# Kernel optimization log

Hardware: AMD Instinct MI355X
Metric: run time of the kernel (lower is better)

## Reference

```python
import jax, jax.numpy as jnp
import numpy as np

W_NBITS = 4
GROUP_SIZE = 128
ELEMS_PER_SAMPLE = 32 // W_NBITS  # 8 nibbles per int32 word
UNPACK_MASK = (1 << W_NBITS) - 1  # 15

M, K, N = 8192, 4096, 11008
KP = K // ELEMS_PER_SAMPLE        # 512 packed rows
NG = K // GROUP_SIZE              # 32 quantization groups


def setup_inputs() -> dict:
    key = jax.random.key(0)
    k1, k2, k3, k4 = jax.random.split(key, 4)
    x = jax.random.normal(k1, (M, K), dtype=jnp.float32)
    # packed 4-bit weights: 8 nibbles per int32 word, packed over the K dim
    W_q = jax.random.randint(k2, (KP, N), 0, 2147483647, dtype=jnp.int32)
    # group-wise scales (small positive) and zero-points (in [0, 15])
    scales = jax.random.uniform(k3, (NG, N), dtype=jnp.float32) * 0.01 + 1e-4
    zeros = jax.random.uniform(k4, (NG, N), dtype=jnp.float32) * float(UNPACK_MASK)
    return {"x": x, "W_q": W_q, "scales": scales, "zeros": zeros}


def _dequantize(W_q, scales, zeros):
    # Unpack 8 consecutive K-rows from each int32 word: [KP, N] -> [KP, 8, N] -> [K, N]
    shifts = (jnp.arange(ELEMS_PER_SAMPLE, dtype=jnp.int32) * W_NBITS)
    nibbles = (W_q[:, None, :] >> shifts[None, :, None]) & UNPACK_MASK
    W = nibbles.reshape(KP * ELEMS_PER_SAMPLE, N).astype(jnp.float32)
    # W_group_mode=3: (w - zero) * scale, group index g = k // group_size
    sf = jnp.repeat(scales, GROUP_SIZE, axis=0)  # [K, N]
    zf = jnp.repeat(zeros, GROUP_SIZE, axis=0)   # [K, N]
    return (W - zf) * sf


def reference(x, W_q, scales, zeros):
    W_dq = _dequantize(W_q, scales, zeros)  # [K, N]
    return jnp.matmul(x, W_dq)              # [M, N]
```

## Files before the change

kernel.cpp:

```cpp
#include <hip/hip_runtime.h>
#include <stdint.h>

#define M_DIM 8192
#define K_DIM 4096
#define N_DIM 11008
#define KP_DIM 512

#define A_PRE_BYTES (67108864ull)
#define B_PRE_BYTES (90177536ull)
#define WS_NEEDED   (A_PRE_BYTES + B_PRE_BYTES)

typedef __attribute__((ext_vector_type(8))) short bf16x8;
typedef __attribute__((ext_vector_type(4))) float f32x4;

__device__ __forceinline__ uint32_t pack2_bf16(float lo, float hi) {
    uint32_t ulo = (__float_as_uint(lo) + 0x8000u) >> 16;
    uint32_t uhi = (__float_as_uint(hi) + 0x8000u) & 0xFFFF0000u;
    return uhi | ulo;
}

__device__ __forceinline__ uint4 dequant_word(uint32_t w, float s, float b) {
    const uint32_t MG = 0x43000000u, MK = 0x000F0000u;
    float f0 = __uint_as_float(((w << 16) & MK) | MG);
    float f1 = __uint_as_float(((w << 12) & MK) | MG);
    float f2 = __uint_as_float(((w <<  8) & MK) | MG);
    float f3 = __uint_as_float(((w <<  4) & MK) | MG);
    float f4 = __uint_as_float(( w        & MK) | MG);
    float f5 = __uint_as_float(((w >>  4) & MK) | MG);
    float f6 = __uint_as_float(((w >>  8) & MK) | MG);
    float f7 = __uint_as_float(((w >> 12) & MK) | MG);
    uint4 o;
    o.x = pack2_bf16(fmaf(f0, s, b), fmaf(f1, s, b));
    o.y = pack2_bf16(fmaf(f2, s, b), fmaf(f3, s, b));
    o.z = pack2_bf16(fmaf(f4, s, b), fmaf(f5, s, b));
    o.w = pack2_bf16(fmaf(f6, s, b), fmaf(f7, s, b));
    return o;
}


__global__ void conv_x(const float* __restrict__ x, uint32_t* __restrict__ Apre) {
    const int c   = blockIdx.x * 256 + threadIdx.x;
    const int row = blockIdx.y;
    const float4* p = reinterpret_cast<const float4*>(x + (size_t)row * K_DIM + c * 8);
    float4 v0 = p[0], v1 = p[1];
    uint4 o;
    o.x = pack2_bf16(v0.x, v0.y);
    o.y = pack2_bf16(v0.z, v0.w);
    o.z = pack2_bf16(v1.x, v1.y);
    o.w = pack2_bf16(v1.z, v1.w);
    const int m_blk = row >> 7, mt = (row >> 4) & 7, lrow = row & 15;
    const int k_blk = c >> 3, ks = (c >> 2) & 1, q = c & 3;
    const int lane  = (q << 4) | lrow;
    const size_t dst = (((size_t)m_blk * 64 + k_blk) * 16 + mt * 2 + ks) * 64 + lane;
    *reinterpret_cast<uint4*>(Apre + dst * 4) = o;
}

__global__ void dequant_w(const int* __restrict__ Wq, const float* __restrict__ scales,
                          const float* __restrict__ zeros, uint32_t* __restrict__ Bpre) {
    const int n  = blockIdx.x * 256 + threadIdx.x;
    const int kp = blockIdx.y;
    const uint32_t w = (uint32_t)Wq[(size_t)kp * N_DIM + n];
    const int g = kp >> 4;
    const float s = scales[(size_t)g * N_DIM + n];
    const float z = zeros[(size_t)g * N_DIM + n];
    const float b = -(128.0f + z) * s;
    uint4 o = dequant_word(w, s, b);
    const int n_blk = n >> 7, nt = (n >> 4) & 7;
    const int k_blk = kp >> 3, ks = (kp >> 2) & 1, q = kp & 3;
    const int lane  = (q << 4) | (n & 15);
    const size_t dst = (((size_t)n_blk * 64 + k_blk) * 16 + nt * 2 + ks) * 64 + lane;
    *reinterpret_cast<uint4*>(Bpre + dst * 4) = o;
}

#define GLD16(g, l) __builtin_amdgcn_global_load_lds(                        \
    (const __attribute__((address_space(1))) uint32_t*)(g),                  \
    (__attribute__((address_space(3))) uint32_t*)(l), 16, 0, 0)

__global__ __launch_bounds__(256, 2)
void gemm_pre(const uint32_t* __restrict__ Apre, const uint32_t* __restrict__ Bpre,
              float* __restrict__ out) {
    __shared__ uint32_t As[4096];
    __shared__ uint32_t Bs[4096];

    const int tid  = threadIdx.x;
    const int lane = tid & 63;
    const int wv   = tid >> 6;
    const int wm   = wv >> 1, wn = wv & 1;
    const int m_blk = blockIdx.x, n_blk = blockIdx.y;

    const uint32_t* ag = Apre + ((size_t)m_blk * 64 * 16 + wv * 4) * 256 + lane * 4;
    const uint32_t* bg = Bpre + ((size_t)n_blk * 64 * 16 + wv * 4) * 256 + lane * 4;
    uint32_t* al = &As[(wv * 4) * 256];
    uint32_t* bl = &Bs[(wv * 4) * 256];

    f32x4 acc[4][4];
#pragma unroll
    for (int mt = 0; mt < 4; ++mt)
#pragma unroll
        for (int nt = 0; nt < 4; ++nt)
            acc[mt][nt] = (f32x4){0.f, 0.f, 0.f, 0.f};

    for (int kb = 0; kb < 64; ++kb) {
#pragma unroll
        for (int i = 0; i < 4; ++i) {
            GLD16(ag + i * 256, al + i * 256);
            GLD16(bg + i * 256, bl + i * 256);
        }
        ag += 4096;
        bg += 4096;
        __syncthreads();

#pragma unroll
        for (int ks = 0; ks < 2; ++ks) {
            bf16x8 af[4], bfr[4];
#pragma unroll
            for (int mt = 0; mt < 4; ++mt)
                af[mt] = *reinterpret_cast<const bf16x8*>(
                    &As[(((wm * 4 + mt) << 1) | ks) * 256 + lane * 4]);
#pragma unroll
            for (int nt = 0; nt < 4; ++nt)
                bfr[nt] = *reinterpret_cast<const bf16x8*>(
                    &Bs[(((wn * 4 + nt) << 1) | ks) * 256 + lane * 4]);
#pragma unroll
            for (int mt = 0; mt < 4; ++mt)
#pragma unroll
                for (int nt = 0; nt < 4; ++nt)
                    acc[mt][nt] = __builtin_amdgcn_mfma_f32_16x16x32_bf16(
                        af[mt], bfr[nt], acc[mt][nt], 0, 0, 0);
        }
        __syncthreads();
    }

    const int colc = lane & 15, qr = lane >> 4;
#pragma unroll
    for (int mt = 0; mt < 4; ++mt) {
#pragma unroll
        for (int nt = 0; nt < 4; ++nt) {
            int row0 = m_blk * 128 + (wm * 4 + mt) * 16 + qr * 4;
            int c    = n_blk * 128 + (wn * 4 + nt) * 16 + colc;
#pragma unroll
            for (int i = 0; i < 4; ++i)
                out[(size_t)(row0 + i) * N_DIM + c] = acc[mt][nt][i];
        }
    }
}

__global__ __launch_bounds__(256, 2)
void qgemm_fused(const float* __restrict__ x, const int* __restrict__ Wq,
                 const float* __restrict__ scales, const float* __restrict__ zeros,
                 float* __restrict__ out) {
    __shared__ uint32_t As[4096];
    __shared__ uint32_t Bs[4096];

    const int tid  = threadIdx.x;
    const int lane = tid & 63;
    const int wv   = tid >> 6;
    const int wm   = wv >> 1, wn = wv & 1;
    const int m0 = blockIdx.x * 128;
    const int n0 = blockIdx.y * 128;
    const int bc  = tid & 127;
    const int brh = tid >> 7;

    int a_row[4], a_col[4], a_dst[4];
#pragma unroll
    for (int j = 0; j < 4; ++j) {
        int sl  = tid + 256 * j;
        int blk = sl >> 6;
        int ln  = sl & 63;
        int mt  = blk >> 1, ks = blk & 1;
        a_row[j] = m0 + mt * 16 + (ln & 15);
        a_col[j] = ks * 32 + (ln >> 4) * 8;
        a_dst[j] = blk * 256 + ln * 4;
    }

    f32x4 acc[4][4];
#pragma unroll
    for (int mt = 0; mt < 4; ++mt)
#pragma unroll
        for (int nt = 0; nt < 4; ++nt)
            acc[mt][nt] = (f32x4){0.f, 0.f, 0.f, 0.f};

    float4   pa[4][2];
    uint32_t pw[4];
    float    s_raw, z_raw;
#pragma unroll
    for (int j = 0; j < 4; ++j) {
        const float4* p = reinterpret_cast<const float4*>(
            x + (size_t)a_row[j] * K_DIM + a_col[j]);
        pa[j][0] = p[0];
        pa[j][1] = p[1];
    }
#pragma unroll
    for (int j = 0; j < 4; ++j) {
        int r = brh * 4 + j;
        pw[j] = (uint32_t)Wq[(size_t)r * N_DIM + n0 + bc];
    }
    s_raw = scales[n0 + bc];
    z_raw = zeros[n0 + bc];

    float sv = 0.f, bv = 0.f;

    for (int kk = 0; kk < K_DIM; kk += 64) {
        if ((kk & 127) == 0) {
            sv = s_raw;
            bv = -(128.0f + z_raw) * s_raw;
        }
#pragma unroll
        for (int j = 0; j < 4; ++j) {
            uint4 o;
            o.x = pack2_bf16(pa[j][0].x, pa[j][0].y);
            o.y = pack2_bf16(pa[j][0].z, pa[j][0].w);
            o.z = pack2_bf16(pa[j][1].x, pa[j][1].y);
            o.w = pack2_bf16(pa[j][1].z, pa[j][1].w);
            *reinterpret_cast<uint4*>(&As[a_dst[j]]) = o;
        }
#pragma unroll
        for (int j = 0; j < 4; ++j) {
            int r  = brh * 4 + j;
            uint4 o = dequant_word(pw[j], sv, bv);
            int ks  = r >> 2, q = r & 3;
            int blk = ((bc >> 4) << 1) | ks;
            *reinterpret_cast<uint4*>(&Bs[blk * 256 + (q * 16 + (bc & 15)) * 4]) = o;
        }
        __syncthreads();

        int kn = kk + 64;
        if (kn < K_DIM) {
#pragma unroll
            for (int j = 0; j < 4; ++j) {
                const float4* p = reinterpret_cast<const float4*>(
                    x + (size_t)a_row[j] * K_DIM + kn + a_col[j]);
                pa[j][0] = p[0];
                pa[j][1] = p[1];
            }
            int kp0 = kn >> 3;
#pragma unroll
            for (int j = 0; j < 4; ++j) {
                int r = brh * 4 + j;
                pw[j] = (uint32_t)Wq[(size_t)(kp0 + r) * N_DIM + n0 + bc];
            }
            if ((kn & 127) == 0) {
                int g = kn >> 7;
                s_raw = scales[(size_t)g * N_DIM + n0 + bc];
                z_raw = zeros[(size_t)g * N_DIM + n0 + bc];
            }
        }

#pragma unroll
        for (int ks = 0; ks < 2; ++ks) {
            bf16x8 af[4], bfr[4];
#pragma unroll
            for (int mt = 0; mt < 4; ++mt)
                af[mt] = *reinterpret_cast<const bf16x8*>(
                    &As[(((wm * 4 + mt) << 1) | ks) * 256 + lane * 4]);
#pragma unroll
            for (int nt = 0; nt < 4; ++nt)
                bfr[nt] = *reinterpret_cast<const bf16x8*>(
                    &Bs[(((wn * 4 + nt) << 1) | ks) * 256 + lane * 4]);
#pragma unroll
            for (int mt = 0; mt < 4; ++mt)
#pragma unroll
                for (int nt = 0; nt < 4; ++nt)
                    acc[mt][nt] = __builtin_amdgcn_mfma_f32_16x16x32_bf16(
                        af[mt], bfr[nt], acc[mt][nt], 0, 0, 0);
        }
        __syncthreads();
    }

    const int colc = lane & 15, qr = lane >> 4;
#pragma unroll
    for (int mt = 0; mt < 4; ++mt) {
#pragma unroll
        for (int nt = 0; nt < 4; ++nt) {
            int row0 = m0 + (wm * 4 + mt) * 16 + qr * 4;
            int c    = n0 + (wn * 4 + nt) * 16 + colc;
#pragma unroll
            for (int i = 0; i < 4; ++i)
                out[(size_t)(row0 + i) * N_DIM + c] = acc[mt][nt][i];
        }
    }
}

extern "C" void kernel_launch(void* const* d_in, const int* in_sizes, int n_in,
                              void* d_out, int out_size, void* d_ws, size_t ws_size,
                              hipStream_t stream) {
    const float* x      = (const float*)d_in[0];
    const int*   Wq     = (const int*)d_in[1];
    const float* scales = (const float*)d_in[2];
    const float* zeros  = (const float*)d_in[3];
    float*       out    = (float*)d_out;

    if (ws_size >= WS_NEEDED) {
        uint32_t* Apre = (uint32_t*)d_ws;
        uint32_t* Bpre = (uint32_t*)((char*)d_ws + A_PRE_BYTES);
        conv_x<<<dim3(2, M_DIM), dim3(256), 0, stream>>>(x, Apre);
        dequant_w<<<dim3(N_DIM / 256, KP_DIM), dim3(256), 0, stream>>>(Wq, scales, zeros, Bpre);
        gemm_pre<<<dim3(M_DIM / 128, N_DIM / 128), dim3(256), 0, stream>>>(Apre, Bpre, out);
    } else {
        qgemm_fused<<<dim3(M_DIM / 128, N_DIM / 128), dim3(256), 0, stream>>>(
            x, Wq, scales, zeros, out);
    }
}
```

Baseline: 1.086 ms.

## Enlarge GEMM tiles to 256x256 with 4-stage LDS pipeline and block swizzle

The pre-packed GEMM moves from 128x128 tiles with 4 waves to 256x256 tiles with 8 waves. K-slices stream through a 4-deep LDS ring using global_load_lds, with explicit vmcnt waits, split barriers and s_setprio around the MFMA bursts. The converters now write the new packed layout linearly. A block-index swizzle groups tiles for L2 reuse. The aim is more data reuse per loaded byte and overlap of loads with MFMA, at the cost of 128KB LDS, higher register pressure and fragile hand-placed waitcnt logic.

```diff
diff --git a/kernel.cpp b/kernel.cpp
--- a/kernel.cpp
+++ b/kernel.cpp
@@ -39,105 +39,139 @@
 
 
 __global__ void conv_x(const float* __restrict__ x, uint32_t* __restrict__ Apre) {
-    const int c   = blockIdx.x * 256 + threadIdx.x;
-    const int row = blockIdx.y;
-    const float4* p = reinterpret_cast<const float4*>(x + (size_t)row * K_DIM + c * 8);
+    const size_t d = (size_t)blockIdx.x * 256 + threadIdx.x;
+    const int lane = (int)(d & 63);
+    const int m16  = (int)((d >> 6) & 15);
+    const int kt   = (int)((d >> 10) & 127);
+    const int mblk = (int)(d >> 17);
+    const int row  = mblk * 256 + m16 * 16 + (lane & 15);
+    const int k    = kt * 32 + (lane >> 4) * 8;
+    const float4* p = reinterpret_cast<const float4*>(x + (size_t)row * K_DIM + k);
     float4 v0 = p[0], v1 = p[1];
     uint4 o;
     o.x = pack2_bf16(v0.x, v0.y);
     o.y = pack2_bf16(v0.z, v0.w);
     o.z = pack2_bf16(v1.x, v1.y);
     o.w = pack2_bf16(v1.z, v1.w);
-    const int m_blk = row >> 7, mt = (row >> 4) & 7, lrow = row & 15;
-    const int k_blk = c >> 3, ks = (c >> 2) & 1, q = c & 3;
-    const int lane  = (q << 4) | lrow;
-    const size_t dst = (((size_t)m_blk * 64 + k_blk) * 16 + mt * 2 + ks) * 64 + lane;
-    *reinterpret_cast<uint4*>(Apre + dst * 4) = o;
+    *reinterpret_cast<uint4*>(Apre + d * 4) = o;
 }
 
 __global__ void dequant_w(const int* __restrict__ Wq, const float* __restrict__ scales,
                           const float* __restrict__ zeros, uint32_t* __restrict__ Bpre) {
-    const int n  = blockIdx.x * 256 + threadIdx.x;
-    const int kp = blockIdx.y;
+    const size_t d = (size_t)blockIdx.x * 256 + threadIdx.x;
+    const int lane = (int)(d & 63);
+    const int n16  = (int)((d >> 6) & 15);
+    const int kt   = (int)((d >> 10) & 127);
+    const int nblk = (int)(d >> 17);
+    const int n    = nblk * 256 + n16 * 16 + (lane & 15);
+    const int kp   = kt * 4 + (lane >> 4);
     const uint32_t w = (uint32_t)Wq[(size_t)kp * N_DIM + n];
     const int g = kp >> 4;
     const float s = scales[(size_t)g * N_DIM + n];
     const float z = zeros[(size_t)g * N_DIM + n];
     const float b = -(128.0f + z) * s;
     uint4 o = dequant_word(w, s, b);
-    const int n_blk = n >> 7, nt = (n >> 4) & 7;
-    const int k_blk = kp >> 3, ks = (kp >> 2) & 1, q = kp & 3;
-    const int lane  = (q << 4) | (n & 15);
-    const size_t dst = (((size_t)n_blk * 64 + k_blk) * 16 + nt * 2 + ks) * 64 + lane;
-    *reinterpret_cast<uint4*>(Bpre + dst * 4) = o;
+    *reinterpret_cast<uint4*>(Bpre + d * 4) = o;
 }
 
 #define GLD16(g, l) __builtin_amdgcn_global_load_lds(                        \
     (const __attribute__((address_space(1))) uint32_t*)(g),                  \
     (__attribute__((address_space(3))) uint32_t*)(l), 16, 0, 0)
 
-__global__ __launch_bounds__(256, 2)
+#define GRID_BLKS 1376
+
+__global__ __launch_bounds__(512, 2)
 void gemm_pre(const uint32_t* __restrict__ Apre, const uint32_t* __restrict__ Bpre,
               float* __restrict__ out) {
-    __shared__ uint32_t As[4096];
-    __shared__ uint32_t Bs[4096];
+    __shared__ uint32_t lds[32768];
 
     const int tid  = threadIdx.x;
     const int lane = tid & 63;
     const int wv   = tid >> 6;
-    const int wm   = wv >> 1, wn = wv & 1;
-    const int m_blk = blockIdx.x, n_blk = blockIdx.y;
-
-    const uint32_t* ag = Apre + ((size_t)m_blk * 64 * 16 + wv * 4) * 256 + lane * 4;
-    const uint32_t* bg = Bpre + ((size_t)n_blk * 64 * 16 + wv * 4) * 256 + lane * 4;
-    uint32_t* al = &As[(wv * 4) * 256];
-    uint32_t* bl = &Bs[(wv * 4) * 256];
-
-    f32x4 acc[4][4];
-#pragma unroll
-    for (int mt = 0; mt < 4; ++mt)
+    const int wm   = wv >> 2;
+    const int wn   = wv & 3;
+
+    const int bid  = blockIdx.x;
+    const int swz  = (bid & 7) * (GRID_BLKS / 8) + (bid >> 3);
+    const int mblk = swz & 31;
+    const int nblk = swz >> 5;
+
+    const uint32_t* ag = Apre + (size_t)mblk * 524288 + (size_t)tid * 4;
+    const uint32_t* bg = Bpre + (size_t)nblk * 524288 + (size_t)tid * 4;
+
+    f32x4 acc[8][4];
+#pragma unroll
+    for (int mt = 0; mt < 8; ++mt)
 #pragma unroll
         for (int nt = 0; nt < 4; ++nt)
             acc[mt][nt] = (f32x4){0.f, 0.f, 0.f, 0.f};
 
-    for (int kb = 0; kb < 64; ++kb) {
-#pragma unroll
-        for (int i = 0; i < 4; ++i) {
-            GLD16(ag + i * 256, al + i * 256);
-            GLD16(bg + i * 256, bl + i * 256);
-        }
-        ag += 4096;
-        bg += 4096;
-        __syncthreads();
-
-#pragma unroll
-        for (int ks = 0; ks < 2; ++ks) {
-            bf16x8 af[4], bfr[4];
-#pragma unroll
-            for (int mt = 0; mt < 4; ++mt)
-                af[mt] = *reinterpret_cast<const bf16x8*>(
-                    &As[(((wm * 4 + mt) << 1) | ks) * 256 + lane * 4]);
-#pragma unroll
-            for (int nt = 0; nt < 4; ++nt)
-                bfr[nt] = *reinterpret_cast<const bf16x8*>(
-                    &Bs[(((wn * 4 + nt) << 1) | ks) * 256 + lane * 4]);
-#pragma unroll
-            for (int mt = 0; mt < 4; ++mt)
-#pragma unroll
-                for (int nt = 0; nt < 4; ++nt)
-                    acc[mt][nt] = __builtin_amdgcn_mfma_f32_16x16x32_bf16(
-                        af[mt], bfr[nt], acc[mt][nt], 0, 0, 0);
-        }
-        __syncthreads();
+#pragma unroll
+    for (int t = 0; t < 3; ++t) {
+        GLD16(ag + t * 4096,        &lds[t * 8192 + wv * 256]);
+        GLD16(ag + t * 4096 + 2048, &lds[t * 8192 + 2048 + wv * 256]);
+        GLD16(bg + t * 4096,        &lds[t * 8192 + 4096 + wv * 256]);
+        GLD16(bg + t * 4096 + 2048, &lds[t * 8192 + 6144 + wv * 256]);
+    }
+    asm volatile("s_waitcnt vmcnt(8)" ::: "memory");
+    __builtin_amdgcn_s_barrier();
+
+    for (int t = 0; t < 128; ++t) {
+        const int buf = t & 3;
+        const uint32_t* Ab = &lds[buf * 8192 + wm * 2048 + lane * 4];
+        const uint32_t* Bb = &lds[buf * 8192 + 4096 + wn * 1024 + lane * 4];
+
+        bf16x8 af[8], bfr[4];
+#pragma unroll
+        for (int mt = 0; mt < 8; ++mt)
+            af[mt] = *reinterpret_cast<const bf16x8*>(Ab + mt * 256);
+        bfr[0] = *reinterpret_cast<const bf16x8*>(Bb);
+        bfr[1] = *reinterpret_cast<const bf16x8*>(Bb + 256);
+        if (t < 125) {
+            const int tn = t + 3, bn = tn & 3;
+            GLD16(ag + tn * 4096,        &lds[bn * 8192 + wv * 256]);
+            GLD16(ag + tn * 4096 + 2048, &lds[bn * 8192 + 2048 + wv * 256]);
+        }
+        __builtin_amdgcn_s_barrier();
+        __builtin_amdgcn_s_setprio(1);
+#pragma unroll
+        for (int mt = 0; mt < 8; ++mt)
+#pragma unroll
+            for (int nt = 0; nt < 2; ++nt)
+                acc[mt][nt] = __builtin_amdgcn_mfma_f32_16x16x32_bf16(
+                    af[mt], bfr[nt], acc[mt][nt], 0, 0, 0);
+        __builtin_amdgcn_s_setprio(0);
+        __builtin_amdgcn_s_barrier();
+
+        bfr[2] = *reinterpret_cast<const bf16x8*>(Bb + 512);
+        bfr[3] = *reinterpret_cast<const bf16x8*>(Bb + 768);
+        if (t < 125) {
+            const int tn = t + 3, bn = tn & 3;
+            GLD16(bg + tn * 4096,        &lds[bn * 8192 + 4096 + wv * 256]);
+            GLD16(bg + tn * 4096 + 2048, &lds[bn * 8192 + 6144 + wv * 256]);
+        }
+        __builtin_amdgcn_s_barrier();
+        __builtin_amdgcn_s_setprio(1);
+#pragma unroll
+        for (int mt = 0; mt < 8; ++mt)
+#pragma unroll
+            for (int nt = 2; nt < 4; ++nt)
+                acc[mt][nt] = __builtin_amdgcn_mfma_f32_16x16x32_bf16(
+                    af[mt], bfr[nt], acc[mt][nt], 0, 0, 0);
+        __builtin_amdgcn_s_setprio(0);
+        if (t < 125)       asm volatile("s_waitcnt vmcnt(8)" ::: "memory");
+        else if (t == 125) asm volatile("s_waitcnt vmcnt(4)" ::: "memory");
+        else if (t == 126) asm volatile("s_waitcnt vmcnt(0)" ::: "memory");
+        __builtin_amdgcn_s_barrier();
     }
 
     const int colc = lane & 15, qr = lane >> 4;
 #pragma unroll
-    for (int mt = 0; mt < 4; ++mt) {
+    for (int mt = 0; mt < 8; ++mt) {
 #pragma unroll
         for (int nt = 0; nt < 4; ++nt) {
-            int row0 = m_blk * 128 + (wm * 4 + mt) * 16 + qr * 4;
-            int c    = n_blk * 128 + (wn * 4 + nt) * 16 + colc;
+            int row0 = mblk * 256 + wm * 128 + mt * 16 + qr * 4;
+            int c    = nblk * 256 + wn * 64 + nt * 16 + colc;
 #pragma unroll
             for (int i = 0; i < 4; ++i)
                 out[(size_t)(row0 + i) * N_DIM + c] = acc[mt][nt][i];
@@ -293,9 +327,9 @@
     if (ws_size >= WS_NEEDED) {
         uint32_t* Apre = (uint32_t*)d_ws;
         uint32_t* Bpre = (uint32_t*)((char*)d_ws + A_PRE_BYTES);
-        conv_x<<<dim3(2, M_DIM), dim3(256), 0, stream>>>(x, Apre);
-        dequant_w<<<dim3(N_DIM / 256, KP_DIM), dim3(256), 0, stream>>>(Wq, scales, zeros, Bpre);
-        gemm_pre<<<dim3(M_DIM / 128, N_DIM / 128), dim3(256), 0, stream>>>(Apre, Bpre, out);
+        conv_x<<<dim3(16384), dim3(256), 0, stream>>>(x, Apre);
+        dequant_w<<<dim3(22016), dim3(256), 0, stream>>>(Wq, scales, zeros, Bpre);
+        gemm_pre<<<dim3(GRID_BLKS), dim3(512), 0, stream>>>(Apre, Bpre, out);
     } else {
         qgemm_fused<<<dim3(M_DIM / 128, N_DIM / 128), dim3(256), 0, stream>>>(
             x, Wq, scales, zeros, out);
```

Result: slower. 1.137 ms (+4.7%).
